# Performance work log

Hardware: AMD Instinct MI355X
Metric: run time of the kernel (lower is better)

## Reference

```python
import jax, jax.numpy as jnp
import numpy as np

B, T, S, D, H, DH = 2, 2048, 2048, 1024, 16, 64
LN_EPS = 1e-5


def setup_inputs() -> dict:
    key = jax.random.key(0)
    ks = jax.random.split(key, 8)
    return {
        "x": jax.random.normal(ks[0], (B, T, D), jnp.float32),
        "context": jax.random.normal(ks[1], (B, S, D), jnp.float32),
        "lookup_table": jax.random.normal(ks[2], (2 * T - 1, DH), jnp.float32),
        "Wq": jax.random.normal(ks[3], (D, H * DH), jnp.float32) * 0.02,
        "Wk": jax.random.normal(ks[4], (D, H * DH), jnp.float32) * 0.02,
        "Wv": jax.random.normal(ks[5], (D, H * DH), jnp.float32) * 0.02,
        "Wo": jax.random.normal(ks[6], (H * DH, D), jnp.float32) * 0.02,
        "bo": jnp.zeros((D,), jnp.float32),
        "gamma": jnp.ones((D,), jnp.float32),
        "beta": jnp.zeros((D,), jnp.float32),
    }


def skew(QE):
    # QE: [B, H, T, 2T-1] -> [B, H, T, T] via pad/reshape relative-position trick
    b, h, t, _ = QE.shape
    QE = jnp.pad(QE, ((0, 0), (0, 0), (0, 0), (0, 1))).reshape(b, h, -1)
    QE = jnp.pad(QE, ((0, 0), (0, 0), (0, t - 1))).reshape(b, h, t + 1, 2 * t - 1)
    return QE[:, :, :t, -t:]


def reference(x, context, lookup_table, Wq, Wk, Wv, Wo, bo, gamma, beta):
    scale = 1.0 / jnp.sqrt(jnp.asarray(DH, x.dtype))
    # pre-layernorm on queries
    mu = jnp.mean(x, axis=-1, keepdims=True)
    var = jnp.var(x, axis=-1, keepdims=True)
    xn = (x - mu) / jnp.sqrt(var + LN_EPS) * gamma + beta
    q = (xn @ Wq).reshape(B, T, H, DH).transpose(0, 2, 1, 3)       # [B,H,T,DH]
    k = (context @ Wk).reshape(B, S, H, DH).transpose(0, 2, 1, 3)  # [B,H,S,DH]
    v = (context @ Wv).reshape(B, S, H, DH).transpose(0, 2, 1, 3)  # [B,H,S,DH]
    score = jnp.einsum("bhtd,bhsd->bhts", q, k) * scale            # [B,H,T,S]
    rel = skew(jnp.einsum("bhtd,ld->bhtl", q, lookup_table))       # [B,H,T,T]
    # NOTE: faithful to original — QK^T gets scaled twice, rel term once
    score = (score + rel) * scale
    attn = jax.nn.softmax(score, axis=-1)
    out = jnp.einsum("bhts,bhsd->bhtd", attn, v)
    out = out.transpose(0, 2, 1, 3).reshape(B, T, H * DH)
    out = out @ Wo + bo
    # dropout=0 (eval); residual uses the layernormed x (as in source)
    return xn + out
```

## Files before the change

### kernel.cpp

```cpp
#include <hip/hip_runtime.h>

#define DEVFN __device__ __forceinline__

typedef __bf16 bf16x8 __attribute__((ext_vector_type(8)));
typedef float f32x4 __attribute__((ext_vector_type(4)));
typedef unsigned short u16;


DEVFN u16 f2bf(float f) {
  unsigned u = __builtin_bit_cast(unsigned, f);
  u += 0x7FFFu + ((u >> 16) & 1u);
  return (u16)(u >> 16);
}

DEVFN f32x4 mfma16(bf16x8 a, bf16x8 b, f32x4 c) {
  return __builtin_amdgcn_mfma_f32_16x16x32_bf16(a, b, c, 0, 0, 0);
}

DEVFN void gl16(const u16* g, u16* l) {
  __builtin_amdgcn_global_load_lds(
      (const __attribute__((address_space(1))) unsigned int*)g,
      (__attribute__((address_space(3))) unsigned int*)l, 16, 0, 0);
}

__global__ __launch_bounds__(256) void ln_kernel(const float* __restrict__ x,
                                                 const float* __restrict__ gamma,
                                                 const float* __restrict__ beta,
                                                 float* __restrict__ xn,
                                                 u16* __restrict__ xnb) {
  int row = blockIdx.x;
  int tid = threadIdx.x;
  const float4* xr = (const float4*)(x + (size_t)row * 1024);
  float4 v = xr[tid];
  float s = v.x + v.y + v.z + v.w;
  float q = v.x * v.x + v.y * v.y + v.z * v.z + v.w * v.w;
#pragma unroll
  for (int m = 1; m < 64; m <<= 1) {
    s += __shfl_xor(s, m);
    q += __shfl_xor(q, m);
  }
  __shared__ float rs[4], rq[4];
  int w = tid >> 6;
  if ((tid & 63) == 0) { rs[w] = s; rq[w] = q; }
  __syncthreads();
  s = rs[0] + rs[1] + rs[2] + rs[3];
  q = rq[0] + rq[1] + rq[2] + rq[3];
  float mean = s * (1.0f / 1024.0f);
  float var = q * (1.0f / 1024.0f) - mean * mean;
  float inv = rsqrtf(var + 1e-5f);
  float4 g = ((const float4*)gamma)[tid];
  float4 bt = ((const float4*)beta)[tid];
  float4 o;
  o.x = (v.x - mean) * inv * g.x + bt.x;
  o.y = (v.y - mean) * inv * g.y + bt.y;
  o.z = (v.z - mean) * inv * g.z + bt.z;
  o.w = (v.w - mean) * inv * g.w + bt.w;
  ((float4*)(xn + (size_t)row * 1024))[tid] = o;
  ushort4 ob;
  ob.x = f2bf(o.x); ob.y = f2bf(o.y); ob.z = f2bf(o.z); ob.w = f2bf(o.w);
  ((ushort4*)(xnb + (size_t)row * 1024))[tid] = ob;
}

__global__ __launch_bounds__(256) void cvt_kernel(const float* __restrict__ in,
                                                  u16* __restrict__ out, int n4) {
  int i = blockIdx.x * 256 + threadIdx.x;
  if (i < n4) {
    float4 v = ((const float4*)in)[i];
    ushort4 o;
    o.x = f2bf(v.x); o.y = f2bf(v.y); o.z = f2bf(v.z); o.w = f2bf(v.w);
    ((ushort4*)out)[i] = o;
  }
}

__global__ __launch_bounds__(256) void transW_kernel(const float* __restrict__ W0,
                                                     const float* __restrict__ W1,
                                                     const float* __restrict__ W2,
                                                     const float* __restrict__ W3,
                                                     u16* __restrict__ Wall) {
  __shared__ float tile[32][33];
  int z = blockIdx.z;
  const float* W = (z == 0) ? W0 : (z == 1) ? W1 : (z == 2) ? W2 : W3;
  float scale = (z == 0) ? 0.18033688011112042f : (z == 1) ? 0.125f : 1.0f;
  u16* Wt = Wall + (size_t)z * 1048576;
  int tx = threadIdx.x, ty = threadIdx.y;
  int x = blockIdx.x * 32 + tx;
  int y0 = blockIdx.y * 32;
#pragma unroll
  for (int j = 0; j < 32; j += 8)
    tile[ty + j][tx] = W[(size_t)(y0 + ty + j) * 1024 + x];
  __syncthreads();
#pragma unroll
  for (int j = 0; j < 32; j += 8)
    Wt[(size_t)(blockIdx.x * 32 + ty + j) * 1024 + y0 + tx] = f2bf(tile[tx][ty + j] * scale);
}

DEVFN void gemm_core(const u16* __restrict__ A, const u16* __restrict__ Bt,
                     u16* Ab, u16* Bb, int row0, int n0, int tid,
                     f32x4 (&acc)[2][4]) {
  int lane = tid & 63, wv = tid >> 6;
  int l16 = lane & 15, lhi = lane >> 4;
  int r8 = lane >> 3, c8 = lane & 7;
  int cx = ((c8 ^ r8) << 3);
  int swz = (l16 & 7) << 3;

  auto stage = [&](int k0) {
#pragma unroll
    for (int i = 0; i < 4; ++i) {
      int rowb = wv * 32 + i * 8;
      gl16(&A[(size_t)(row0 + rowb + r8) * 1024 + k0 + cx], &Ab[rowb * 64]);
    }
#pragma unroll
    for (int i = 0; i < 2; ++i) {
      int rowb = wv * 16 + i * 8;
      gl16(&Bt[(size_t)(n0 + rowb + r8) * 1024 + k0 + cx], &Bb[rowb * 64]);
    }
  };

  stage(0);
  asm volatile("s_waitcnt vmcnt(0)" ::: "memory");
  __syncthreads();
  for (int kk = 0; kk < 16; ++kk) {
    __builtin_amdgcn_s_setprio(1);
#pragma unroll
    for (int ks = 0; ks < 2; ++ks) {
      bf16x8 af[2], bfr[4];
#pragma unroll
      for (int mi = 0; mi < 2; ++mi) {
        int row = wv * 32 + mi * 16 + l16;
        af[mi] = *(const bf16x8*)&Ab[row * 64 + ((ks * 32 + lhi * 8) ^ swz)];
      }
#pragma unroll
      for (int ni = 0; ni < 4; ++ni) {
        int row = ni * 16 + l16;
        bfr[ni] = *(const bf16x8*)&Bb[row * 64 + ((ks * 32 + lhi * 8) ^ swz)];
      }
#pragma unroll
      for (int mi = 0; mi < 2; ++mi)
#pragma unroll
        for (int ni = 0; ni < 4; ++ni)
          acc[mi][ni] = mfma16(af[mi], bfr[ni], acc[mi][ni]);
    }
    __builtin_amdgcn_s_setprio(0);
    if (kk < 15) {
      __syncthreads();
      stage((kk + 1) * 64);
      asm volatile("s_waitcnt vmcnt(0)" ::: "memory");
      __syncthreads();
    }
  }
}

__global__ __launch_bounds__(256, 4) void qkv_kernel(const u16* __restrict__ xnb,
                                                     const u16* __restrict__ ctxb,
                                                     const u16* __restrict__ Wall,
                                                     u16* __restrict__ qb,
                                                     u16* __restrict__ kb,
                                                     u16* __restrict__ vtb) {
  __shared__ __align__(16) u16 Ab[128 * 64];
  __shared__ __align__(16) u16 Bb[64 * 64];
  int z = blockIdx.z;
  const u16* A = (z == 0) ? xnb : ctxb;
  const u16* Bt = Wall + (size_t)z * 1048576;
  int row0 = blockIdx.x * 128, n0 = blockIdx.y * 64;
  f32x4 acc[2][4] = {};
  gemm_core(A, Bt, Ab, Bb, row0, n0, threadIdx.x, acc);
  int tid = threadIdx.x, lane = tid & 63, wv = tid >> 6;
  int l16 = lane & 15, lhi = lane >> 4;
  u16* qk = (z == 0) ? qb : kb;
#pragma unroll
  for (int mi = 0; mi < 2; ++mi)
#pragma unroll
    for (int ni = 0; ni < 4; ++ni)
#pragma unroll
      for (int r = 0; r < 4; ++r) {
        int m = row0 + wv * 32 + mi * 16 + lhi * 4 + r;
        int n = n0 + ni * 16 + l16;
        int b = m >> 11, t = m & 2047, h = n >> 6, dh = n & 63;
        u16 val = f2bf(acc[mi][ni][r]);
        if (z < 2)
          qk[(size_t)((b * 16 + h) * 2048 + t) * 64 + dh] = val;
        else
          vtb[(size_t)((b * 16 + h) * 64 + dh) * 2048 + t] = val;
      }
}

__global__ __launch_bounds__(256, 4) void oproj_kernel(const u16* __restrict__ attnb,
                                                       const u16* __restrict__ Wall,
                                                       const float* __restrict__ bias,
                                                       const float* __restrict__ resid,
                                                       float* __restrict__ outF) {
  __shared__ __align__(16) u16 Ab[128 * 64];
  __shared__ __align__(16) u16 Bb[64 * 64];
  const u16* Bt = Wall + (size_t)3 * 1048576;
  int row0 = blockIdx.x * 128, n0 = blockIdx.y * 64;
  f32x4 acc[2][4] = {};
  gemm_core(attnb, Bt, Ab, Bb, row0, n0, threadIdx.x, acc);
  int tid = threadIdx.x, lane = tid & 63, wv = tid >> 6;
  int l16 = lane & 15, lhi = lane >> 4;
#pragma unroll
  for (int mi = 0; mi < 2; ++mi)
#pragma unroll
    for (int ni = 0; ni < 4; ++ni)
#pragma unroll
      for (int r = 0; r < 4; ++r) {
        int m = row0 + wv * 32 + mi * 16 + lhi * 4 + r;
        int n = n0 + ni * 16 + l16;
        outF[(size_t)m * 1024 + n] = acc[mi][ni][r] + bias[n] + resid[(size_t)m * 1024 + n];
      }
}

__global__ __launch_bounds__(256, 4) void flash_kernel(
    const u16* __restrict__ Qg, const u16* __restrict__ Kg,
    const u16* __restrict__ Vtg, const u16* __restrict__ Lb,
    u16* __restrict__ Og) {
  constexpr int T = 2048, H = 16;
  int p = blockIdx.x;
  int bid = (p & 7) * 128 + (p >> 3);
  int qb = bid & 31, h = (bid >> 5) & 15, b = bid >> 9;
  int tid = threadIdx.x;
  int lane = tid & 63, w = tid >> 6;
  int l16 = lane & 15, lhi = lane >> 4;

  __shared__ __align__(16) u16 Klds[2][64 * 64];
  __shared__ __align__(16) u16 Vt[2][64 * 64];
  __shared__ __align__(16) u16 Plds[4][16 * 64];

  const u16* qbase = Qg + (size_t)(b * H + h) * T * 64;
  const u16* kbase = Kg + (size_t)(b * H + h) * T * 64;
  const u16* vtbase = Vtg + (size_t)(b * H + h) * 64 * 2048;

  int i0w = qb * 64 + w * 16;
  bf16x8 aq[2];
  aq[0] = *(const bf16x8*)&qbase[(i0w + l16) * 64 + lhi * 8];
  aq[1] = *(const bf16x8*)&qbase[(i0w + l16) * 64 + 32 + lhi * 8];

  f32x4 accO[4] = {};
  float mrun[4], lsum[4];
#pragma unroll
  for (int r = 0; r < 4; ++r) { mrun[r] = -1e30f; lsum[r] = 0.0f; }

  int bandbase = T - 16 - i0w;

  int r8 = lane >> 3, c8 = lane & 7;
  int cx = ((c8 ^ r8) << 3);
  int swz = (l16 & 7) << 3;

  auto stage = [&](int bufi, int j0) {
#pragma unroll
    for (int i = 0; i < 2; ++i) {
      int rowb = w * 16 + i * 8;
      gl16(&kbase[(size_t)(j0 + rowb + r8) * 64 + cx], &Klds[bufi][rowb * 64]);
    }
#pragma unroll
    for (int i = 0; i < 2; ++i) {
      int rowb = w * 16 + i * 8;
      gl16(&vtbase[(size_t)(rowb + r8) * 2048 + j0 + cx], &Vt[bufi][rowb * 64]);
    }
  };

  const u16* lp = Lb + (size_t)(bandbase + l16) * 64 + lhi * 8;

  f32x4 eC = {};
#pragma unroll
  for (int ks = 0; ks < 2; ++ks)
    eC = mfma16(aq[ks], *(const bf16x8*)&lp[ks * 32], eC);

  stage(0, 0);

  const float THR = 11.541560327111707f;

  for (int kt = 0; kt < 32; ++kt) {
    __syncthreads();
    int cb = kt & 1;
    if (kt < 31) stage(cb ^ 1, (kt + 1) * 64);

    const u16* lpt = lp + (size_t)kt * 4096;
    f32x4 accE[5];
    accE[0] = eC;
#pragma unroll
    for (int c = 1; c < 5; ++c) accE[c] = f32x4{0.f, 0.f, 0.f, 0.f};
#pragma unroll
    for (int ks = 0; ks < 2; ++ks) {
      bf16x8 bl[4];
#pragma unroll
      for (int c = 1; c < 5; ++c)
        bl[c - 1] = *(const bf16x8*)&lpt[c * 1024 + ks * 32];
      __builtin_amdgcn_s_setprio(1);
#pragma unroll
      for (int c = 1; c < 5; ++c) accE[c] = mfma16(aq[ks], bl[c - 1], accE[c]);
      __builtin_amdgcn_s_setprio(0);
    }
    eC = accE[4];

    f32x4 accS[4] = {};
    __builtin_amdgcn_s_setprio(1);
#pragma unroll
    for (int ks = 0; ks < 2; ++ks)
#pragma unroll
      for (int kb = 0; kb < 4; ++kb) {
        int row = kb * 16 + l16;
        bf16x8 bk = *(const bf16x8*)&Klds[cb][row * 64 + ((ks * 32 + lhi * 8) ^ swz)];
        accS[kb] = mfma16(aq[ks], bk, accS[kb]);
      }
    __builtin_amdgcn_s_setprio(0);

    float sc[4][4];
    float lm[4];
    bool need = false;
#pragma unroll
    for (int r = 0; r < 4; ++r) {
      int m = lhi * 4 + r;
      int srcl = lhi * 16 + ((l16 - m + 15) & 15);
      bool lo = (l16 <= m);
      float e[5];
#pragma unroll
      for (int c = 0; c < 5; ++c) e[c] = __shfl(accE[c][r], srcl);
#pragma unroll
      for (int kb = 0; kb < 4; ++kb) sc[r][kb] = accS[kb][r] + (lo ? e[kb] : e[kb + 1]);
      lm[r] = fmaxf(fmaxf(sc[r][0], sc[r][1]), fmaxf(sc[r][2], sc[r][3]));
      need |= (lm[r] > mrun[r] + THR);
    }
    if (__ballot(need)) {
#pragma unroll
      for (int r = 0; r < 4; ++r) {
        float tm = lm[r];
        tm = fmaxf(tm, __shfl_xor(tm, 1));
        tm = fmaxf(tm, __shfl_xor(tm, 2));
        tm = fmaxf(tm, __shfl_xor(tm, 4));
        tm = fmaxf(tm, __shfl_xor(tm, 8));
        float mnew = fmaxf(mrun[r], tm);
        float al = exp2f(mrun[r] - mnew);
        mrun[r] = mnew;
        lsum[r] *= al;
#pragma unroll
        for (int dt = 0; dt < 4; ++dt) accO[dt][r] *= al;
      }
    }
#pragma unroll
    for (int r = 0; r < 4; ++r) {
      int m = lhi * 4 + r;
      int swm = (m & 7) << 3;
      float mm = mrun[r];
      float pv0 = exp2f(sc[r][0] - mm);
      float pv1 = exp2f(sc[r][1] - mm);
      float pv2 = exp2f(sc[r][2] - mm);
      float pv3 = exp2f(sc[r][3] - mm);
      lsum[r] += (pv0 + pv1) + (pv2 + pv3);
      unsigned pk01, pk23;
      asm("v_cvt_pk_bf16_f32 %0, %1, %2" : "=v"(pk01) : "v"(pv0), "v"(pv1));
      asm("v_cvt_pk_bf16_f32 %0, %1, %2" : "=v"(pk23) : "v"(pv2), "v"(pv3));
      Plds[w][m * 64 + ((l16) ^ swm)] = (u16)pk01;
      Plds[w][m * 64 + ((16 + l16) ^ swm)] = (u16)(pk01 >> 16);
      Plds[w][m * 64 + ((32 + l16) ^ swm)] = (u16)pk23;
      Plds[w][m * 64 + ((48 + l16) ^ swm)] = (u16)(pk23 >> 16);
    }

    __builtin_amdgcn_s_setprio(1);
#pragma unroll
    for (int ks = 0; ks < 2; ++ks) {
      bf16x8 ap = *(const bf16x8*)&Plds[w][l16 * 64 + ((ks * 32 + lhi * 8) ^ swz)];
#pragma unroll
      for (int dt = 0; dt < 4; ++dt) {
        int row = dt * 16 + l16;
        bf16x8 bv = *(const bf16x8*)&Vt[cb][row * 64 + ((ks * 32 + lhi * 8) ^ swz)];
        accO[dt] = mfma16(ap, bv, accO[dt]);
      }
    }
    __builtin_amdgcn_s_setprio(0);
  }

#pragma unroll
  for (int r = 0; r < 4; ++r) {
    float l = lsum[r];
    l += __shfl_xor(l, 1);
    l += __shfl_xor(l, 2);
    l += __shfl_xor(l, 4);
    l += __shfl_xor(l, 8);
    lsum[r] = 1.0f / l;
  }
#pragma unroll
  for (int dt = 0; dt < 4; ++dt)
#pragma unroll
    for (int r = 0; r < 4; ++r) {
      int i = i0w + lhi * 4 + r;
      int col = h * 64 + dt * 16 + l16;
      Og[(size_t)(b * T + i) * 1024 + col] = f2bf(accO[dt][r] * lsum[r]);
    }
}

extern "C" void kernel_launch(void* const* d_in, const int* in_sizes, int n_in,
                              void* d_out, int out_size, void* d_ws, size_t ws_size,
                              hipStream_t stream) {
  const float* x = (const float*)d_in[0];
  const float* ctx = (const float*)d_in[1];
  const float* Ltab = (const float*)d_in[2];
  const float* Wq = (const float*)d_in[3];
  const float* Wk = (const float*)d_in[4];
  const float* Wv = (const float*)d_in[5];
  const float* Wo = (const float*)d_in[6];
  const float* bo = (const float*)d_in[7];
  const float* gamma = (const float*)d_in[8];
  const float* beta = (const float*)d_in[9];
  float* out = (float*)d_out;

  size_t off = 0;
  auto take = [&](size_t bytes) {
    void* p = (char*)d_ws + off;
    off += (bytes + 255) & ~(size_t)255;
    return p;
  };
  u16* xnb = (u16*)take(8388608);
  u16* ctxb = (u16*)take(8388608);
  u16* Lb = (u16*)take(4095 * 64 * 2);
  u16* Wall = (u16*)take(4 * 2097152);
  u16* qbuf = (u16*)take(8388608);
  u16* kbuf = (u16*)take(8388608);
  u16* vtbuf = (u16*)take(8388608);
  u16* attnb = (u16*)take(8388608);

  ln_kernel<<<dim3(4096), dim3(256), 0, stream>>>(x, gamma, beta, out, xnb);
  cvt_kernel<<<dim3(4096), dim3(256), 0, stream>>>(ctx, ctxb, 1048576);
  cvt_kernel<<<dim3(256), dim3(256), 0, stream>>>(Ltab, Lb, 65520);
  transW_kernel<<<dim3(32, 32, 4), dim3(32, 8), 0, stream>>>(Wq, Wk, Wv, Wo, Wall);
  qkv_kernel<<<dim3(32, 16, 3), dim3(256), 0, stream>>>(xnb, ctxb, Wall, qbuf, kbuf, vtbuf);
  flash_kernel<<<dim3(1024), dim3(256), 0, stream>>>(qbuf, kbuf, vtbuf, Lb, attnb);
  oproj_kernel<<<dim3(32, 16), dim3(256), 0, stream>>>(attnb, Wall, bo, out, out);
}
```

Baseline: 227.5 us.

## Fuse K and V projections sharing context tiles; reorder rel-pos MFMAs in flash loop

Splits the combined QKV launch into a Q projection kernel and a fused K/V kernel. The fused kernel stages each context tile once and multiplies it against both Wk and Wv, halving context loads for those projections. In the flash kernel, the lookup-table loads are issued up front and their MFMAs are moved after the QK^T MFMAs so the global load latency can overlap. This adds an extra launch and more registers and LDS per block in the K/V kernel, which may lower occupancy.

```diff
diff --git a/kernel.cpp b/kernel.cpp
--- a/kernel.cpp
+++ b/kernel.cpp
@@ -150,23 +150,16 @@
   }
 }
 
-__global__ __launch_bounds__(256, 4) void qkv_kernel(const u16* __restrict__ xnb,
-                                                     const u16* __restrict__ ctxb,
-                                                     const u16* __restrict__ Wall,
-                                                     u16* __restrict__ qb,
-                                                     u16* __restrict__ kb,
-                                                     u16* __restrict__ vtb) {
+__global__ __launch_bounds__(256, 4) void qproj_kernel(const u16* __restrict__ xnb,
+                                                       const u16* __restrict__ Wall,
+                                                       u16* __restrict__ qb) {
   __shared__ __align__(16) u16 Ab[128 * 64];
   __shared__ __align__(16) u16 Bb[64 * 64];
-  int z = blockIdx.z;
-  const u16* A = (z == 0) ? xnb : ctxb;
-  const u16* Bt = Wall + (size_t)z * 1048576;
   int row0 = blockIdx.x * 128, n0 = blockIdx.y * 64;
   f32x4 acc[2][4] = {};
-  gemm_core(A, Bt, Ab, Bb, row0, n0, threadIdx.x, acc);
+  gemm_core(xnb, Wall, Ab, Bb, row0, n0, threadIdx.x, acc);
   int tid = threadIdx.x, lane = tid & 63, wv = tid >> 6;
   int l16 = lane & 15, lhi = lane >> 4;
-  u16* qk = (z == 0) ? qb : kb;
 #pragma unroll
   for (int mi = 0; mi < 2; ++mi)
 #pragma unroll
@@ -176,11 +169,88 @@
         int m = row0 + wv * 32 + mi * 16 + lhi * 4 + r;
         int n = n0 + ni * 16 + l16;
         int b = m >> 11, t = m & 2047, h = n >> 6, dh = n & 63;
-        u16 val = f2bf(acc[mi][ni][r]);
-        if (z < 2)
-          qk[(size_t)((b * 16 + h) * 2048 + t) * 64 + dh] = val;
-        else
-          vtb[(size_t)((b * 16 + h) * 64 + dh) * 2048 + t] = val;
+        qb[(size_t)((b * 16 + h) * 2048 + t) * 64 + dh] = f2bf(acc[mi][ni][r]);
+      }
+}
+
+__global__ __launch_bounds__(256, 4) void kv_kernel(const u16* __restrict__ ctxb,
+                                                    const u16* __restrict__ Wall,
+                                                    u16* __restrict__ kbuf,
+                                                    u16* __restrict__ vtb) {
+  __shared__ __align__(16) u16 Ab[128 * 64];
+  __shared__ __align__(16) u16 Bk[64 * 64];
+  __shared__ __align__(16) u16 Bv[64 * 64];
+  const u16* Wk = Wall + 1048576;
+  const u16* Wv = Wall + 2097152;
+  int tid = threadIdx.x;
+  int lane = tid & 63, wv = tid >> 6;
+  int l16 = lane & 15, lhi = lane >> 4;
+  int r8 = lane >> 3, c8 = lane & 7;
+  int cx = ((c8 ^ r8) << 3);
+  int swz = (l16 & 7) << 3;
+  int row0 = blockIdx.x * 128, n0 = blockIdx.y * 64;
+
+  auto stage = [&](int k0) {
+#pragma unroll
+    for (int i = 0; i < 4; ++i) {
+      int rowb = wv * 32 + i * 8;
+      gl16(&ctxb[(size_t)(row0 + rowb + r8) * 1024 + k0 + cx], &Ab[rowb * 64]);
+    }
+    {
+      int rowb = wv * 16;
+      gl16(&Wk[(size_t)(n0 + rowb + r8) * 1024 + k0 + cx], &Bk[rowb * 64]);
+      gl16(&Wk[(size_t)(n0 + rowb + 8 + r8) * 1024 + k0 + cx], &Bk[(rowb + 8) * 64]);
+      gl16(&Wv[(size_t)(n0 + rowb + r8) * 1024 + k0 + cx], &Bv[rowb * 64]);
+      gl16(&Wv[(size_t)(n0 + rowb + 8 + r8) * 1024 + k0 + cx], &Bv[(rowb + 8) * 64]);
+    }
+  };
+
+  f32x4 accK[2][4] = {};
+  f32x4 accV[2][4] = {};
+  stage(0);
+  asm volatile("s_waitcnt vmcnt(0)" ::: "memory");
+  __syncthreads();
+  for (int kk = 0; kk < 16; ++kk) {
+    __builtin_amdgcn_s_setprio(1);
+#pragma unroll
+    for (int ks = 0; ks < 2; ++ks) {
+      bf16x8 af[2];
+#pragma unroll
+      for (int mi = 0; mi < 2; ++mi) {
+        int row = wv * 32 + mi * 16 + l16;
+        af[mi] = *(const bf16x8*)&Ab[row * 64 + ((ks * 32 + lhi * 8) ^ swz)];
+      }
+#pragma unroll
+      for (int ni = 0; ni < 4; ++ni) {
+        int row = ni * 16 + l16;
+        bf16x8 bk = *(const bf16x8*)&Bk[row * 64 + ((ks * 32 + lhi * 8) ^ swz)];
+        accK[0][ni] = mfma16(af[0], bk, accK[0][ni]);
+        accK[1][ni] = mfma16(af[1], bk, accK[1][ni]);
+        bf16x8 bv = *(const bf16x8*)&Bv[row * 64 + ((ks * 32 + lhi * 8) ^ swz)];
+        accV[0][ni] = mfma16(af[0], bv, accV[0][ni]);
+        accV[1][ni] = mfma16(af[1], bv, accV[1][ni]);
+      }
+    }
+    __builtin_amdgcn_s_setprio(0);
+    if (kk < 15) {
+      __syncthreads();
+      stage((kk + 1) * 64);
+      asm volatile("s_waitcnt vmcnt(0)" ::: "memory");
+      __syncthreads();
+    }
+  }
+
+#pragma unroll
+  for (int mi = 0; mi < 2; ++mi)
+#pragma unroll
+    for (int ni = 0; ni < 4; ++ni)
+#pragma unroll
+      for (int r = 0; r < 4; ++r) {
+        int m = row0 + wv * 32 + mi * 16 + lhi * 4 + r;
+        int n = n0 + ni * 16 + l16;
+        int b = m >> 11, t = m & 2047, h = n >> 6, dh = n & 63;
+        kbuf[(size_t)((b * 16 + h) * 2048 + t) * 64 + dh] = f2bf(accK[mi][ni][r]);
+        vtb[(size_t)((b * 16 + h) * 64 + dh) * 2048 + t] = f2bf(accV[mi][ni][r]);
       }
 }
 
@@ -275,22 +345,12 @@
     if (kt < 31) stage(cb ^ 1, (kt + 1) * 64);
 
     const u16* lpt = lp + (size_t)kt * 4096;
-    f32x4 accE[5];
-    accE[0] = eC;
-#pragma unroll
-    for (int c = 1; c < 5; ++c) accE[c] = f32x4{0.f, 0.f, 0.f, 0.f};
-#pragma unroll
-    for (int ks = 0; ks < 2; ++ks) {
-      bf16x8 bl[4];
+    bf16x8 bl[8];
+#pragma unroll
+    for (int ks = 0; ks < 2; ++ks)
 #pragma unroll
       for (int c = 1; c < 5; ++c)
-        bl[c - 1] = *(const bf16x8*)&lpt[c * 1024 + ks * 32];
-      __builtin_amdgcn_s_setprio(1);
-#pragma unroll
-      for (int c = 1; c < 5; ++c) accE[c] = mfma16(aq[ks], bl[c - 1], accE[c]);
-      __builtin_amdgcn_s_setprio(0);
-    }
-    eC = accE[4];
+        bl[ks * 4 + c - 1] = *(const bf16x8*)&lpt[c * 1024 + ks * 32];
 
     f32x4 accS[4] = {};
     __builtin_amdgcn_s_setprio(1);
@@ -302,7 +362,18 @@
         bf16x8 bk = *(const bf16x8*)&Klds[cb][row * 64 + ((ks * 32 + lhi * 8) ^ swz)];
         accS[kb] = mfma16(aq[ks], bk, accS[kb]);
       }
+
+    f32x4 accE[5];
+    accE[0] = eC;
+#pragma unroll
+    for (int c = 1; c < 5; ++c) accE[c] = f32x4{0.f, 0.f, 0.f, 0.f};
+#pragma unroll
+    for (int ks = 0; ks < 2; ++ks)
+#pragma unroll
+      for (int c = 1; c < 5; ++c)
+        accE[c] = mfma16(aq[ks], bl[ks * 4 + c - 1], accE[c]);
     __builtin_amdgcn_s_setprio(0);
+    eC = accE[4];
 
     float sc[4][4];
     float lm[4];
@@ -422,7 +493,8 @@
   cvt_kernel<<<dim3(4096), dim3(256), 0, stream>>>(ctx, ctxb, 1048576);
   cvt_kernel<<<dim3(256), dim3(256), 0, stream>>>(Ltab, Lb, 65520);
   transW_kernel<<<dim3(32, 32, 4), dim3(32, 8), 0, stream>>>(Wq, Wk, Wv, Wo, Wall);
-  qkv_kernel<<<dim3(32, 16, 3), dim3(256), 0, stream>>>(xnb, ctxb, Wall, qbuf, kbuf, vtbuf);
+  qproj_kernel<<<dim3(32, 16), dim3(256), 0, stream>>>(xnb, Wall, qbuf);
+  kv_kernel<<<dim3(32, 16), dim3(256), 0, stream>>>(ctxb, Wall, kbuf, vtbuf);
   flash_kernel<<<dim3(1024), dim3(256), 0, stream>>>(qbuf, kbuf, vtbuf, Lb, attnb);
   oproj_kernel<<<dim3(32, 16), dim3(256), 0, stream>>>(attnb, Wall, bo, out, out);
 }
```

Result: slower. 244.4 us (+7.4%).

## Stage relative-position table band through LDS and drop K/V double buffering

Applied to the files above, without the earlier changes.

The relative-position lookup rows are now loaded cooperatively into shared memory with async global-to-LDS copies, so each wave reads its band from LDS. Before, every wave read them directly from global memory with overlapping per-wave reads. K/V staging is reduced to a single buffer: tiles are loaded at the top of each iteration with a barrier before and after the compute. This cuts redundant global traffic and frees shared memory, but it gives up the overlap of the next tile's loads with current compute and adds a second barrier per iteration.

```diff
diff --git a/kernel.cpp b/kernel.cpp
--- a/kernel.cpp
+++ b/kernel.cpp
@@ -221,15 +221,17 @@
   int lane = tid & 63, w = tid >> 6;
   int l16 = lane & 15, lhi = lane >> 4;
 
-  __shared__ __align__(16) u16 Klds[2][64 * 64];
-  __shared__ __align__(16) u16 Vt[2][64 * 64];
+  __shared__ __align__(16) u16 Klds[64 * 64];
+  __shared__ __align__(16) u16 Vt[64 * 64];
+  __shared__ __align__(16) u16 Llds[128 * 64];
   __shared__ __align__(16) u16 Plds[4][16 * 64];
 
   const u16* qbase = Qg + (size_t)(b * H + h) * T * 64;
   const u16* kbase = Kg + (size_t)(b * H + h) * T * 64;
   const u16* vtbase = Vtg + (size_t)(b * H + h) * 64 * 2048;
 
-  int i0w = qb * 64 + w * 16;
+  int i0b = qb * 64;
+  int i0w = i0b + w * 16;
   bf16x8 aq[2];
   aq[0] = *(const bf16x8*)&qbase[(i0w + l16) * 64 + lhi * 8];
   aq[1] = *(const bf16x8*)&qbase[(i0w + l16) * 64 + 32 + lhi * 8];
@@ -240,69 +242,69 @@
   for (int r = 0; r < 4; ++r) { mrun[r] = -1e30f; lsum[r] = 0.0f; }
 
   int bandbase = T - 16 - i0w;
+  int ubase0 = T - 64 - i0b;
+  int uoff = 48 - 16 * w;
 
   int r8 = lane >> 3, c8 = lane & 7;
   int cx = ((c8 ^ r8) << 3);
   int swz = (l16 & 7) << 3;
 
-  auto stage = [&](int bufi, int j0) {
+  auto stage = [&](int j0) {
 #pragma unroll
     for (int i = 0; i < 2; ++i) {
       int rowb = w * 16 + i * 8;
-      gl16(&kbase[(size_t)(j0 + rowb + r8) * 64 + cx], &Klds[bufi][rowb * 64]);
+      gl16(&kbase[(size_t)(j0 + rowb + r8) * 64 + cx], &Klds[rowb * 64]);
     }
 #pragma unroll
     for (int i = 0; i < 2; ++i) {
       int rowb = w * 16 + i * 8;
-      gl16(&vtbase[(size_t)(rowb + r8) * 2048 + j0 + cx], &Vt[bufi][rowb * 64]);
+      gl16(&vtbase[(size_t)(rowb + r8) * 2048 + j0 + cx], &Vt[rowb * 64]);
+    }
+#pragma unroll
+    for (int i = 0; i < 4; ++i) {
+      int rowb = w * 32 + i * 8;
+      gl16(&Lb[(size_t)(ubase0 + j0 + rowb + r8) * 64 + cx], &Llds[rowb * 64]);
     }
   };
 
   const u16* lp = Lb + (size_t)(bandbase + l16) * 64 + lhi * 8;
-
   f32x4 eC = {};
 #pragma unroll
   for (int ks = 0; ks < 2; ++ks)
     eC = mfma16(aq[ks], *(const bf16x8*)&lp[ks * 32], eC);
 
-  stage(0, 0);
-
   const float THR = 11.541560327111707f;
 
   for (int kt = 0; kt < 32; ++kt) {
+    int j0 = kt * 64;
+    stage(j0);
     __syncthreads();
-    int cb = kt & 1;
-    if (kt < 31) stage(cb ^ 1, (kt + 1) * 64);
-
-    const u16* lpt = lp + (size_t)kt * 4096;
+
+    f32x4 accS[4] = {};
+    __builtin_amdgcn_s_setprio(1);
+#pragma unroll
+    for (int ks = 0; ks < 2; ++ks)
+#pragma unroll
+      for (int kb = 0; kb < 4; ++kb) {
+        int row = kb * 16 + l16;
+        bf16x8 bk = *(const bf16x8*)&Klds[row * 64 + ((ks * 32 + lhi * 8) ^ swz)];
+        accS[kb] = mfma16(aq[ks], bk, accS[kb]);
+      }
+
     f32x4 accE[5];
     accE[0] = eC;
 #pragma unroll
     for (int c = 1; c < 5; ++c) accE[c] = f32x4{0.f, 0.f, 0.f, 0.f};
 #pragma unroll
-    for (int ks = 0; ks < 2; ++ks) {
-      bf16x8 bl[4];
-#pragma unroll
-      for (int c = 1; c < 5; ++c)
-        bl[c - 1] = *(const bf16x8*)&lpt[c * 1024 + ks * 32];
-      __builtin_amdgcn_s_setprio(1);
-#pragma unroll
-      for (int c = 1; c < 5; ++c) accE[c] = mfma16(aq[ks], bl[c - 1], accE[c]);
-      __builtin_amdgcn_s_setprio(0);
-    }
+    for (int ks = 0; ks < 2; ++ks)
+#pragma unroll
+      for (int c = 1; c < 5; ++c) {
+        int urow = uoff + c * 16 + l16;
+        bf16x8 bl = *(const bf16x8*)&Llds[urow * 64 + ((ks * 32 + lhi * 8) ^ swz)];
+        accE[c] = mfma16(aq[ks], bl, accE[c]);
+      }
+    __builtin_amdgcn_s_setprio(0);
     eC = accE[4];
-
-    f32x4 accS[4] = {};
-    __builtin_amdgcn_s_setprio(1);
-#pragma unroll
-    for (int ks = 0; ks < 2; ++ks)
-#pragma unroll
-      for (int kb = 0; kb < 4; ++kb) {
-        int row = kb * 16 + l16;
-        bf16x8 bk = *(const bf16x8*)&Klds[cb][row * 64 + ((ks * 32 + lhi * 8) ^ swz)];
-        accS[kb] = mfma16(aq[ks], bk, accS[kb]);
-      }
-    __builtin_amdgcn_s_setprio(0);
 
     float sc[4][4];
     float lm[4];
@@ -362,11 +364,12 @@
 #pragma unroll
       for (int dt = 0; dt < 4; ++dt) {
         int row = dt * 16 + l16;
-        bf16x8 bv = *(const bf16x8*)&Vt[cb][row * 64 + ((ks * 32 + lhi * 8) ^ swz)];
+        bf16x8 bv = *(const bf16x8*)&Vt[row * 64 + ((ks * 32 + lhi * 8) ^ swz)];
         accO[dt] = mfma16(ap, bv, accO[dt]);
       }
     }
     __builtin_amdgcn_s_setprio(0);
+    __syncthreads();
   }
 
 #pragma unroll
```

New measurement: 210.4 us. 7.5% less time.
